# Performance work log

Measured on AMD Instinct MI355X. Metric: run time of the kernel, lower is better.

## Reference

```python
import jax, jax.numpy as jnp
import numpy as np

N = 50000
E = 500000
R = 8
IN_DIM = 128
HID = 128
OUT = 128
NUM_GRAPHS = 64
EPS_BN = 1e-5


def _glorot(key, shape):
    fan_in, fan_out = shape[-2], shape[-1]
    lim = np.sqrt(6.0 / (fan_in + fan_out))
    return jax.random.uniform(key, shape, jnp.float32, -lim, lim)


def setup_inputs() -> dict:
    key = jax.random.key(0)
    ks = jax.random.split(key, 24)
    x = jax.random.normal(ks[0], (N, IN_DIM), jnp.float32)
    edge_index = jax.random.randint(ks[1], (2, E), 0, N, jnp.int64)
    edge_type = jax.random.randint(ks[2], (E,), 0, R, jnp.int64)
    batch = jnp.sort(jax.random.randint(ks[3], (N,), 0, NUM_GRAPHS, jnp.int64))
    d = {
        "x": x, "edge_index": edge_index, "edge_type": edge_type, "batch": batch,
        # RGCN layer 1 (in->hid): per-relation weights, root weight, bias
        "W1": _glorot(ks[4], (R, IN_DIM, HID)), "root1": _glorot(ks[5], (IN_DIM, HID)), "b1": jnp.zeros((HID,), jnp.float32),
        "W2": _glorot(ks[6], (R, HID, HID)), "root2": _glorot(ks[7], (HID, HID)), "b2": jnp.zeros((HID,), jnp.float32),
        "W3": _glorot(ks[8], (R, HID, HID)), "root3": _glorot(ks[9], (HID, HID)), "b3": jnp.zeros((HID,), jnp.float32),
        # BatchNorm affine params
        "g1": jnp.ones((HID,), jnp.float32), "beta1": jnp.zeros((HID,), jnp.float32),
        "g2": jnp.ones((HID,), jnp.float32), "beta2": jnp.zeros((HID,), jnp.float32),
        # attention MLP: hid -> hid//2 -> 1
        "A1": _glorot(ks[10], (HID, HID // 2)), "a1": jnp.zeros((HID // 2,), jnp.float32),
        "A2": _glorot(ks[11], (HID // 2, 1)), "a2": jnp.zeros((1,), jnp.float32),
        # combiner MLP: 2*hid -> hid -> out
        "C1": _glorot(ks[12], (2 * HID, HID)), "c1": jnp.zeros((HID,), jnp.float32),
        "C2": _glorot(ks[13], (HID, OUT)), "c2": jnp.zeros((OUT,), jnp.float32),
    }
    return d


def rgcn_conv(h, src, dst, etype, W, root, bias):
    # relation-wise gather -> mean-aggregate per (dst, relation) -> transform
    seg = dst * R + etype                                   # [E]
    msg = h[src]                                            # [E, d_in] gather
    agg = jax.ops.segment_sum(msg, seg, num_segments=N * R) # [N*R, d_in]
    cnt = jax.ops.segment_sum(jnp.ones((seg.shape[0],), h.dtype), seg, num_segments=N * R)
    agg = agg / jnp.maximum(cnt, 1.0)[:, None]              # mean aggregation (PyG default)
    agg = agg.reshape(N, R, -1)
    out = jnp.einsum('nri,rio->no', agg, W) + h @ root + bias
    return out


def batch_norm(h, gamma, beta):
    mu = jnp.mean(h, axis=0, keepdims=True)
    var = jnp.mean((h - mu) ** 2, axis=0, keepdims=True)
    return (h - mu) * jax.lax.rsqrt(var + EPS_BN) * gamma + beta


def lrelu(h):
    return jax.nn.leaky_relu(h, 0.1)


def reference(x, edge_index, edge_type, batch, W1, root1, b1, W2, root2, b2,
              W3, root3, b3, g1, beta1, g2, beta2, A1, a1, A2, a2, C1, c1, C2, c2):
    src, dst = edge_index[0], edge_index[1]
    h = rgcn_conv(x, src, dst, edge_type, W1, root1, b1)
    h = lrelu(batch_norm(h, g1, beta1))
    h = rgcn_conv(h, src, dst, edge_type, W2, root2, b2)
    h = lrelu(batch_norm(h, g2, beta2))
    node_emb = rgcn_conv(h, src, dst, edge_type, W3, root3, b3)  # [N, HID]

    # attention pooling: scores softmax-ed over ALL nodes (dim=0, as in source)
    scores = lrelu(node_emb @ A1 + a1) @ A2 + a2                 # [N, 1]
    attn = jax.nn.softmax(scores, axis=0)                        # [N, 1]
    global_emb = jax.ops.segment_sum(node_emb * attn, batch, num_segments=NUM_GRAPHS)

    combined = jnp.concatenate([node_emb, global_emb[batch]], axis=1)  # [N, 2*HID]
    final = lrelu(combined @ C1 + c1) @ C2 + c2                  # [N, OUT]
    norm = jnp.linalg.norm(final, axis=1, keepdims=True)
    return final / jnp.maximum(norm, 1e-12)
```

## Files before the change

kernel.cpp:

```cpp
#include <hip/hip_runtime.h>
#include <hip/hip_bf16.h>

typedef unsigned int u32;
typedef unsigned short u16;
typedef __bf16 bf16_t;
typedef bf16_t bf16x8 __attribute__((ext_vector_type(8)));
typedef float f32x4 __attribute__((ext_vector_type(4)));

constexpr int NN = 50000;
constexpr int EE = 500000;
constexpr int RR = 8;
constexpr int NKEY = RR * NN;
constexpr int PAIR_B = (NKEY + 511) / 512;

constexpr int WX_A1T = 0;
constexpr int WX_C1T = 8192;
constexpr int WX_C2T = 40960;
constexpr int WX_A2  = 57344;
constexpr int WX_a1  = 57408;
constexpr int WX_c1  = 57472;
constexpr int WX_c2  = 57600;
constexpr int WX_a2s = 57728;
constexpr int WX_TOT = 57729;

__device__ __forceinline__ float bf2f(u32 v){
  union { u32 u; float f; } x; x.u = (v & 0xFFFFu) << 16; return x.f;
}
__device__ __forceinline__ u16 f2bf(float f){
  union { u32 u; float f; } x; x.f = f;
  u32 r = x.u + 0x7FFFu + ((x.u >> 16) & 1u);
  return (u16)(r >> 16);
}
__device__ __forceinline__ float lrelu(float x){ return x > 0.f ? x : 0.1f * x; }
__device__ __forceinline__ float ldf(const void* p, int i, u32 fm){
  return fm ? ((const float*)p)[i] : bf2f(((const u16*)p)[i]);
}
__device__ __forceinline__ void gl_lds16(const u16* g, u16* l){
  __builtin_amdgcn_global_load_lds((const __attribute__((address_space(1))) u32*)g,
                                   (__attribute__((address_space(3))) u32*)l, 16, 0, 0);
}
__device__ __forceinline__ bf16x8 cvt8(float4 a, float4 b){
  union { bf16x8 v; u16 s[8]; } r;
  r.s[0]=f2bf(a.x); r.s[1]=f2bf(a.y); r.s[2]=f2bf(a.z); r.s[3]=f2bf(a.w);
  r.s[4]=f2bf(b.x); r.s[5]=f2bf(b.y); r.s[6]=f2bf(b.z); r.s[7]=f2bf(b.w);
  return r.v;
}

__global__ void k_fdetect(const void* x, u32* md){
  __shared__ u32 c;
  if (threadIdx.x == 0) c = 0;
  __syncthreads();
  const u16* p = (const u16*)x;
  u32 loc = 0;
  for (int j = 0; j < 16; j++){
    u16 v = p[threadIdx.x * 16 + j];
    u32 e = (v >> 7) & 0xFF;
    if (e >= 0xFD) loc++;
  }
  atomicAdd(&c, loc);
  __syncthreads();
  if (threadIdx.x == 0) md[0] = (c >= 4) ? 1u : 0u;
}
__global__ void k_idetect(const void* et, u32* md){
  __shared__ u32 c;
  if (threadIdx.x == 0) c = 0;
  __syncthreads();
  const int* p = (const int*)et;
  u32 loc = 0;
  for (int j = 0; j < 8; j++){
    int idx = 2 * (threadIdx.x * 8 + j) + 1;
    if (p[idx] != 0) loc++;
  }
  atomicAdd(&c, loc);
  __syncthreads();
  if (threadIdx.x == 0) md[1] = (c == 0) ? 1u : 0u;
}

__global__ void k_icvt(const void* ei, const void* et, const void* bat,
                       int* ei_c, int* et_c, int* bat_c, const u32* md){
  u32 im = md[1];
  int i = blockIdx.x * 256 + threadIdx.x;
  if (i < 2 * EE){
    const int* p = (const int*)ei;
    ei_c[i] = im ? p[2 * i] : p[i];
  } else if (i < 3 * EE){
    int j = i - 2 * EE;
    const int* p = (const int*)et;
    et_c[j] = im ? p[2 * j] : p[j];
  } else if (i < 3 * EE + NN){
    int j = i - 3 * EE;
    const int* p = (const int*)bat;
    bat_c[j] = im ? p[2 * j] : p[j];
  }
}

__global__ void k_xcvt(const void* x, u16* xb, const u32* md, u32* flags){
  u32 fm = md[0];
  int i4 = (blockIdx.x * 256 + threadIdx.x) * 4;
  if (i4 >= NN * 128) return;
  float v[4];
  if (fm){
    float4 f = *(const float4*)((const float*)x + i4);
    v[0]=f.x; v[1]=f.y; v[2]=f.z; v[3]=f.w;
  } else {
    uint2 u = *(const uint2*)((const u16*)x + i4);
    v[0]=bf2f(u.x); v[1]=bf2f(u.x>>16); v[2]=bf2f(u.y); v[3]=bf2f(u.y>>16);
  }
  bool bad = false;
  u16 o[4];
  for (int j = 0; j < 4; j++){
    if (v[j] != v[j]){ bad = true; v[j] = 0.f; }
    o[j] = f2bf(v[j]);
  }
  unsigned long long bal = __ballot(bad);
  if (bal && (threadIdx.x & 63) == 0) atomicOr(flags, 2u);
  uint2 st;
  st.x = (u32)o[0] | ((u32)o[1] << 16);
  st.y = (u32)o[2] | ((u32)o[3] << 16);
  *(uint2*)(xb + i4) = st;
}

__global__ void k_wcat(const void* W1, const void* r1, const void* W2, const void* r2,
                       const void* W3, const void* r3, u16* wcatT, const u32* md, u32* flags){
  u32 fm = md[0];
  int idx = blockIdx.x * 256 + threadIdx.x;
  if (idx >= 3 * 128 * 1152) return;
  int L = idx / (128 * 1152);
  int rem = idx % (128 * 1152);
  int n = rem / 1152, k = rem % 1152;
  const void* W  = (L == 0) ? W1 : ((L == 1) ? W2 : W3);
  const void* rt = (L == 0) ? r1 : ((L == 1) ? r2 : r3);
  float v;
  if (k < 1024){
    int r = k & 7, c = k >> 3;
    v = ldf(W, (r * 128 + c) * 128 + n, fm);
  } else {
    v = ldf(rt, (k - 1024) * 128 + n, fm);
  }
  if (v != v){ v = 0.f; atomicOr(flags, 2u); }
  wcatT[idx] = f2bf(v);
}

__global__ void k_wext(const void* A1, const void* a1, const void* A2, const void* a2,
                       const void* C1, const void* c1, const void* C2, const void* c2,
                       u16* wext, const u32* md){
  u32 fm = md[0];
  int idx = blockIdx.x * 256 + threadIdx.x;
  if (idx >= WX_TOT) return;
  float v;
  if (idx < WX_C1T){
    int n = idx >> 7, k = idx & 127;
    v = ldf(A1, k * 64 + n, fm);
  } else if (idx < WX_C2T){
    int j = idx - WX_C1T; int n = j >> 8, k = j & 255;
    v = ldf(C1, k * 128 + n, fm);
  } else if (idx < WX_A2){
    int j = idx - WX_C2T; int n = j >> 7, k = j & 127;
    v = ldf(C2, k * 128 + n, fm);
  } else if (idx < WX_a1){ v = ldf(A2, idx - WX_A2, fm); }
  else if (idx < WX_c1){ v = ldf(a1, idx - WX_a1, fm); }
  else if (idx < WX_c2){ v = ldf(c1, idx - WX_c1, fm); }
  else if (idx < WX_a2s){ v = ldf(c2, idx - WX_c2, fm); }
  else { v = ldf(a2, 0, fm); }
  wext[idx] = f2bf(v);
}

__global__ void k_count3(const int* __restrict__ ei, const int* __restrict__ et, u32* __restrict__ cnt){
  int e = blockIdx.x * 256 + threadIdx.x;
  if (e >= EE) return;
  atomicAdd(&cnt[ei[EE + e] * RR + et[e]], 1u);
}
__global__ void k_pairA(const u32* __restrict__ cnt, u32* __restrict__ blockSum){
  __shared__ u32 sd[256];
  int b = blockIdx.x, t = threadIdx.x;
  u32 s = 0;
  for (int j = 0; j < 2; j++){
    int key = b * 512 + t * 2 + j;
    if (key < NKEY) s += cnt[key];
  }
  sd[t] = s; __syncthreads();
  for (int off = 128; off; off >>= 1){ if (t < off) sd[t] += sd[t + off]; __syncthreads(); }
  if (t == 0) blockSum[b] = sd[0];
}
__global__ void k_pairB(const u32* __restrict__ blockSum, u32* __restrict__ blockBase){
  int lane = threadIdx.x;
  u32 loc[13]; u32 s = 0;
  for (int j = 0; j < 13; j++){
    int b = lane * 13 + j;
    u32 v = (b < PAIR_B) ? blockSum[b] : 0u;
    loc[j] = s; s += v;
  }
  u32 tot = s;
  for (int off = 1; off < 64; off <<= 1){
    u32 x = __shfl_up(tot, off);
    if (lane >= off) tot += x;
  }
  u32 excl = tot - s;
  for (int j = 0; j < 13; j++){
    int b = lane * 13 + j;
    if (b < PAIR_B) blockBase[b] = excl + loc[j];
  }
}
__global__ void k_pairC(const u32* __restrict__ cnt, const u32* __restrict__ blockBase,
                        u32* __restrict__ pairStart, u32* __restrict__ cursor){
  __shared__ u32 sd[256];
  int b = blockIdx.x, t = threadIdx.x;
  int k0 = b * 512 + t * 2;
  u32 v0 = 0, v1 = 0;
  if (k0 < NKEY) v0 = cnt[k0];
  if (k0 + 1 < NKEY) v1 = cnt[k0 + 1];
  sd[t] = v0 + v1; __syncthreads();
  for (int off = 1; off < 256; off <<= 1){
    u32 x = (t >= off) ? sd[t - off] : 0u;
    __syncthreads();
    sd[t] += x;
    __syncthreads();
  }
  u32 excl = sd[t] - (v0 + v1);
  u32 base = blockBase[b] + excl;
  if (k0 < NKEY){ pairStart[k0] = base; cursor[k0] = 0u; }
  if (k0 + 1 < NKEY){ pairStart[k0 + 1] = base + v0; cursor[k0 + 1] = 0u; }
  if (k0 + 1 == NKEY - 1) pairStart[NKEY] = base + v0 + v1;
}
__global__ void k_sort3(const int* __restrict__ ei, const int* __restrict__ et,
                        const u32* __restrict__ pairStart, u32* __restrict__ cursor,
                        u32* __restrict__ src_s){
  int e = blockIdx.x * 256 + threadIdx.x;
  if (e >= EE) return;
  int r = et[e], d = ei[EE + e];
  u32 key = (u32)d * RR + (u32)r;
  u32 p = pairStart[key] + atomicAdd(&cursor[key], 1u);
  src_s[p] = (u32)ei[e];
}

__global__ __launch_bounds__(256) void k_agg(const u16* __restrict__ h,
                                             const u32* __restrict__ pairStart,
                                             const u32* __restrict__ src_s,
                                             u16* __restrict__ agg){
  int d = blockIdx.x * 4 + (threadIdx.x >> 6);
  if (d >= NN) return;
  int lane = threadIdx.x & 63;
  const uint4* p4 = (const uint4*)(pairStart + d * 8);
  uint4 q0 = p4[0], q1 = p4[1];
  u32 ps[9];
  ps[0]=q0.x; ps[1]=q0.y; ps[2]=q0.z; ps[3]=q0.w;
  ps[4]=q1.x; ps[5]=q1.y; ps[6]=q1.z; ps[7]=q1.w;
  ps[8]=pairStart[d * 8 + 8];
  u32 jb = ps[0], je = ps[8];
  u32 pre = 0;
  if (jb + lane < je) pre = src_s[jb + lane];
  const u16* hb = h + lane * 2;
  u32 ou[8] = {0,0,0,0,0,0,0,0};
  #pragma unroll
  for (int r = 0; r < 8; r++){
    u32 s = ps[r], e = ps[r + 1];
    float a0 = 0.f, a1 = 0.f, b0 = 0.f, b1 = 0.f;
    u32 j = s;
    for (; j + 1 < e; j += 2){
      u32 i0 = j - jb;
      u32 s0 = (i0 < 64) ? __shfl(pre, (int)i0) : src_s[j];
      u32 s1 = (i0 + 1 < 64) ? __shfl(pre, (int)(i0 + 1)) : src_s[j + 1];
      u32 v0 = *(const u32*)(hb + (size_t)s0 * 128);
      u32 v1 = *(const u32*)(hb + (size_t)s1 * 128);
      a0 += bf2f(v0); a1 += bf2f(v0 >> 16);
      b0 += bf2f(v1); b1 += bf2f(v1 >> 16);
    }
    if (j < e){
      u32 i0 = j - jb;
      u32 s0 = (i0 < 64) ? __shfl(pre, (int)i0) : src_s[j];
      u32 v0 = *(const u32*)(hb + (size_t)s0 * 128);
      a0 += bf2f(v0); a1 += bf2f(v0 >> 16);
    }
    a0 += b0; a1 += b1;
    int c = (int)(e - s);
    float sc = 1.0f / (float)max(c, 1);
    u32 m0 = (u32)f2bf(a0 * sc), m1 = (u32)f2bf(a1 * sc);
    ou[r >> 1]       |= m0 << ((r & 1) * 16);
    ou[4 + (r >> 1)] |= m1 << ((r & 1) * 16);
  }
  uint4* dst = (uint4*)(agg + (size_t)d * 1024 + lane * 16);
  dst[0] = make_uint4(ou[0], ou[1], ou[2], ou[3]);
  dst[1] = make_uint4(ou[4], ou[5], ou[6], ou[7]);
}

__global__ __launch_bounds__(256) void k_gemm_big(const u16* __restrict__ h,
                                                  const u16* __restrict__ agg,
                                                  const u16* __restrict__ wT,
                                                  const void* __restrict__ bias,
                                                  float* __restrict__ out, const u32* md,
                                                  float* __restrict__ stats, int do_stats){
  __shared__ u16 As[64][64];
  __shared__ u16 Bs[128][64];
  u32 fm = md[0];
  int m0 = blockIdx.x * 64;
  int tid = threadIdx.x;
  int w = tid >> 6, lane = tid & 63, qd = lane >> 4, l16 = lane & 15;

  int rin = lane >> 3;
  int sc8 = (lane & 7) ^ rin;

  const u16* agA[2]; const u16* hA[2]; u16* ldsA[2];
  #pragma unroll
  for (int i = 0; i < 2; i++){
    int row = (w * 2 + i) * 8 + rin;
    int node = m0 + row; if (node > NN - 1) node = NN - 1;
    agA[i] = agg + (size_t)node * 1024 + sc8 * 8;
    hA[i]  = h + (size_t)node * 128 + sc8 * 8;
    ldsA[i] = &As[(w * 2 + i) * 8][0];
  }
  const u16* wB[4]; u16* ldsB[4];
  #pragma unroll
  for (int i = 0; i < 4; i++){
    int row = (w * 4 + i) * 8 + rin;
    wB[i] = wT + (size_t)row * 1152 + sc8 * 8;
    ldsB[i] = &Bs[(w * 4 + i) * 8][0];
  }

  f32x4 acc[8];
  #pragma unroll
  for (int j = 0; j < 8; j++) acc[j] = (f32x4){0.f,0.f,0.f,0.f};

  int sw = (l16 & 7) << 3;
  for (int k0 = 0; k0 < 1152; k0 += 64){
    __syncthreads();
    if (k0 < 1024){
      gl_lds16(agA[0] + k0, ldsA[0]);
      gl_lds16(agA[1] + k0, ldsA[1]);
    } else {
      gl_lds16(hA[0] + (k0 - 1024), ldsA[0]);
      gl_lds16(hA[1] + (k0 - 1024), ldsA[1]);
    }
    #pragma unroll
    for (int i = 0; i < 4; i++) gl_lds16(wB[i] + k0, ldsB[i]);
    __syncthreads();
    #pragma unroll
    for (int kk = 0; kk < 64; kk += 32){
      bf16x8 a = *(const bf16x8*)(&As[w * 16 + l16][(kk + qd * 8) ^ sw]);
      #pragma unroll
      for (int ct = 0; ct < 8; ct++){
        bf16x8 b = *(const bf16x8*)(&Bs[ct * 16 + l16][(kk + qd * 8) ^ sw]);
        acc[ct] = __builtin_amdgcn_mfma_f32_16x16x32_bf16(a, b, acc[ct], 0, 0, 0);
      }
    }
  }

  float sarr[8], s2arr[8];
  #pragma unroll
  for (int ct = 0; ct < 8; ct++){
    int col = ct * 16 + l16;
    float bv = ldf(bias, col, fm);
    float s = 0.f, s2 = 0.f;
    int rbase = m0 + w * 16 + qd * 4;
    #pragma unroll
    for (int rg = 0; rg < 4; rg++){
      int node = rbase + rg;
      if (node < NN){
        float v = acc[ct][rg] + bv;
        out[(size_t)node * 128 + col] = v;
        s += v; s2 += v * v;
      }
    }
    s  += __shfl_xor(s, 16);  s  += __shfl_xor(s, 32);
    s2 += __shfl_xor(s2, 16); s2 += __shfl_xor(s2, 32);
    sarr[ct] = s; s2arr[ct] = s2;
  }
  if (do_stats){
    float* red = (float*)&As[0][0];
    __syncthreads();
    if (qd == 0){
      #pragma unroll
      for (int ct = 0; ct < 8; ct++){
        red[w * 256 + ct * 16 + l16] = sarr[ct];
        red[w * 256 + 128 + ct * 16 + l16] = s2arr[ct];
      }
    }
    __syncthreads();
    if (tid < 256){
      float v = red[tid] + red[256 + tid] + red[512 + tid] + red[768 + tid];
      unsafeAtomicAdd(&stats[tid], v);
    }
  }
}

__global__ void k_bnapply(const float* __restrict__ out, const float* __restrict__ stats,
                          const void* __restrict__ g, const void* __restrict__ beta,
                          u16* __restrict__ hout, const u32* md, u32* flags, u32 layerbit){
  u32 fm = md[0];
  int idx = (blockIdx.x * 256 + threadIdx.x) * 4;
  if (idx >= NN * 128) return;
  int col = idx & 127;
  float4 v = *(const float4*)(out + idx);
  float vv[4] = {v.x, v.y, v.z, v.w};
  bool bad = false;
  u16 o[4];
  for (int j = 0; j < 4; j++){
    int c = col + j;
    float mu = stats[c] * (1.0f / NN);
    float var = fmaxf(stats[128 + c] * (1.0f / NN) - mu * mu, 0.f);
    float sc = ldf(g, c, fm) * rsqrtf(var + 1e-5f);
    float sh = ldf(beta, c, fm) - mu * sc;
    float r = vv[j] * sc + sh;
    if (r != r || sc != sc){ bad = true; r = 0.f; }
    o[j] = f2bf(lrelu(r));
  }
  unsigned long long bal = __ballot(bad);
  if (bal && (threadIdx.x & 63) == 0) atomicOr(flags, layerbit);
  uint2 st;
  st.x = (u32)o[0] | ((u32)o[1] << 16);
  st.y = (u32)o[2] | ((u32)o[3] << 16);
  *(uint2*)(hout + idx) = st;
}

__global__ __launch_bounds__(256) void k_scores_mfma(const float* __restrict__ emb,
                                                     const u16* __restrict__ wext,
                                                     float* __restrict__ scores, u32* smax){
  int m0 = blockIdx.x * 64;
  int tid = threadIdx.x;
  int w = tid >> 6, lane = tid & 63, qd = lane >> 4, l16 = lane & 15;
  int na = m0 + w * 16 + l16; if (na > NN - 1) na = NN - 1;
  const float* arow = emb + (size_t)na * 128;
  f32x4 acc[4];
  #pragma unroll
  for (int j = 0; j < 4; j++) acc[j] = (f32x4){0.f,0.f,0.f,0.f};
  #pragma unroll
  for (int k0 = 0; k0 < 4; k0++){
    float4 f0 = *(const float4*)(arow + k0 * 32 + qd * 8);
    float4 f1 = *(const float4*)(arow + k0 * 32 + qd * 8 + 4);
    bf16x8 a = cvt8(f0, f1);
    #pragma unroll
    for (int ct = 0; ct < 4; ct++){
      bf16x8 b = *(const bf16x8*)(wext + WX_A1T + (size_t)(ct * 16 + l16) * 128 + k0 * 32 + qd * 8);
      acc[ct] = __builtin_amdgcn_mfma_f32_16x16x32_bf16(a, b, acc[ct], 0, 0, 0);
    }
  }
  float a1v[4], a2v[4];
  #pragma unroll
  for (int ct = 0; ct < 4; ct++){
    a1v[ct] = bf2f(wext[WX_a1 + ct * 16 + l16]);
    a2v[ct] = bf2f(wext[WX_A2 + ct * 16 + l16]);
  }
  float a2s = bf2f(wext[WX_a2s]);
  float bm = -1e30f;
  #pragma unroll
  for (int rg = 0; rg < 4; rg++){
    float s = 0.f;
    #pragma unroll
    for (int ct = 0; ct < 4; ct++)
      s += lrelu(acc[ct][rg] + a1v[ct]) * a2v[ct];
    s += __shfl_xor(s, 1); s += __shfl_xor(s, 2);
    s += __shfl_xor(s, 4); s += __shfl_xor(s, 8);
    int row = m0 + w * 16 + qd * 4 + rg;
    float sf = s + a2s;
    if (row < NN){
      bm = fmaxf(bm, sf);
      if (l16 == 0) scores[row] = sf;
    }
  }
  bm = fmaxf(bm, __shfl_xor(bm, 16));
  bm = fmaxf(bm, __shfl_xor(bm, 32));
  if (lane == 0) atomicMax(smax, (bm >= -1e29f) ?
      ((__float_as_uint(bm) & 0x80000000u) ? ~__float_as_uint(bm) : (__float_as_uint(bm) | 0x80000000u)) : 0u);
}

__device__ __forceinline__ float funmap(u32 m){
  union{u32 u; float f;} x;
  x.u = (m & 0x80000000u) ? (m ^ 0x80000000u) : ~m;
  return x.f;
}

__global__ void k_expsum(const float* __restrict__ scores, const u32* smax,
                         float* __restrict__ attnw, float* ssum, u32* flags){
  float mx = funmap(*smax);
  int gid = blockIdx.x * 256 + threadIdx.x;
  if (mx != mx){ if (gid == 0) atomicOr(flags, 32u); mx = 0.f; }
  float s = 0.f;
  bool bad = false;
  for (int i = gid; i < NN; i += 256 * 128){
    float e = __expf(scores[i] - mx);
    if (e != e){ bad = true; e = 0.f; }
    attnw[i] = e; s += e;
  }
  unsigned long long bal = __ballot(bad);
  if (bal && (threadIdx.x & 63) == 0) atomicOr(flags, 32u);
  for (int off = 32; off; off >>= 1) s += __shfl_down(s, off);
  if ((threadIdx.x & 63) == 0) unsafeAtomicAdd(ssum, s);
}

constexpr int POOL_CHUNK = 32;
__global__ __launch_bounds__(128) void k_pool(const float* __restrict__ emb,
                                              const float* __restrict__ attnw,
                                              const float* __restrict__ ssum,
                                              const int* __restrict__ batch,
                                              float* __restrict__ gemb, u32* flags){
  int t = threadIdx.x;
  int n0 = blockIdx.x * POOL_CHUNK;
  if (n0 >= NN) return;
  int n1 = min(n0 + POOL_CHUNK, NN);
  float sv = *ssum;
  bool bad = !(sv > 0.f) || (sv != sv);
  if (bad && t == 0 && blockIdx.x == 0) atomicOr(flags, 64u);
  float rs = bad ? 0.f : 1.0f / sv;
  int cur = batch[n0];
  float acc = 0.f;
  for (int n = n0; n < n1; n++){
    int b = batch[n];
    if (b != cur){ unsafeAtomicAdd(&gemb[cur * 128 + t], acc * rs); acc = 0.f; cur = b; }
    acc += emb[(size_t)n * 128 + t] * attnw[n];
  }
  unsafeAtomicAdd(&gemb[cur * 128 + t], acc * rs);
}

__global__ void k_gembC(const float* __restrict__ gemb, const u16* __restrict__ wext,
                        float* __restrict__ gembC){
  int idx = blockIdx.x * 256 + threadIdx.x;
  if (idx >= 64 * 128) return;
  int g = idx >> 7, n = idx & 127;
  const float* gr = gemb + g * 128;
  const u16* wr = wext + WX_C1T + (size_t)n * 256 + 128;
  float s = 0.f;
  #pragma unroll 8
  for (int k = 0; k < 128; k++) s += gr[k] * bf2f(wr[k]);
  gembC[idx] = s + bf2f(wext[WX_c1 + n]);
}

__global__ __launch_bounds__(256) void k_final_mfma(const float* __restrict__ emb,
                                                    const float* __restrict__ gembC,
                                                    const int* __restrict__ batch,
                                                    const u16* __restrict__ wext,
                                                    void* __restrict__ outp,
                                                    const u32* md){
  __shared__ u16 Hs[64][136];
  u32 fm = md[0];
  int m0 = blockIdx.x * 64;
  int tid = threadIdx.x;
  int w = tid >> 6, lane = tid & 63, qd = lane >> 4, l16 = lane & 15;
  int na = m0 + w * 16 + l16; if (na > NN - 1) na = NN - 1;
  const float* arow = emb + (size_t)na * 128;

  f32x4 acc[8];
  #pragma unroll
  for (int j = 0; j < 8; j++) acc[j] = (f32x4){0.f,0.f,0.f,0.f};
  #pragma unroll
  for (int k0 = 0; k0 < 4; k0++){
    float4 f0 = *(const float4*)(arow + k0 * 32 + qd * 8);
    float4 f1 = *(const float4*)(arow + k0 * 32 + qd * 8 + 4);
    bf16x8 a = cvt8(f0, f1);
    #pragma unroll
    for (int ct = 0; ct < 8; ct++){
      bf16x8 b = *(const bf16x8*)(wext + WX_C1T + (size_t)(ct * 16 + l16) * 256 + k0 * 32 + qd * 8);
      acc[ct] = __builtin_amdgcn_mfma_f32_16x16x32_bf16(a, b, acc[ct], 0, 0, 0);
    }
  }
  int rbase = w * 16 + qd * 4;
  int gg[4];
  #pragma unroll
  for (int rg = 0; rg < 4; rg++){
    int node = m0 + rbase + rg; if (node > NN - 1) node = NN - 1;
    gg[rg] = batch[node];
  }
  #pragma unroll
  for (int ct = 0; ct < 8; ct++){
    int col = ct * 16 + l16;
    #pragma unroll
    for (int rg = 0; rg < 4; rg++){
      float h = acc[ct][rg] + gembC[gg[rg] * 128 + col];
      Hs[rbase + rg][col] = f2bf(lrelu(h));
    }
  }
  __syncthreads();
  f32x4 acc2[8];
  #pragma unroll
  for (int j = 0; j < 8; j++) acc2[j] = (f32x4){0.f,0.f,0.f,0.f};
  #pragma unroll
  for (int k0 = 0; k0 < 4; k0++){
    bf16x8 a = *(const bf16x8*)(&Hs[w * 16 + l16][k0 * 32 + qd * 8]);
    #pragma unroll
    for (int ct = 0; ct < 8; ct++){
      bf16x8 b = *(const bf16x8*)(wext + WX_C2T + (size_t)(ct * 16 + l16) * 128 + k0 * 32 + qd * 8);
      acc2[ct] = __builtin_amdgcn_mfma_f32_16x16x32_bf16(a, b, acc2[ct], 0, 0, 0);
    }
  }
  float c2v[8];
  #pragma unroll
  for (int ct = 0; ct < 8; ct++) c2v[ct] = bf2f(wext[WX_c2 + ct * 16 + l16]);
  #pragma unroll
  for (int rg = 0; rg < 4; rg++){
    float ss = 0.f;
    #pragma unroll
    for (int ct = 0; ct < 8; ct++){
      float o = acc2[ct][rg] + c2v[ct];
      ss += o * o;
    }
    ss += __shfl_xor(ss, 1); ss += __shfl_xor(ss, 2);
    ss += __shfl_xor(ss, 4); ss += __shfl_xor(ss, 8);
    float sc = 1.0f / fmaxf(sqrtf(ss), 1e-12f);
    int row = m0 + rbase + rg;
    if (row < NN){
      if (fm){
        float* op = (float*)outp;
        #pragma unroll
        for (int ct = 0; ct < 8; ct++)
          op[(size_t)row * 128 + ct * 16 + l16] = (acc2[ct][rg] + c2v[ct]) * sc;
      } else {
        u16* op = (u16*)outp;
        #pragma unroll
        for (int ct = 0; ct < 8; ct++)
          op[(size_t)row * 128 + ct * 16 + l16] = f2bf((acc2[ct][rg] + c2v[ct]) * sc);
      }
    }
  }
}

__global__ void k_diag(const u32* pairStart, const u32* flags, const u32* md, void* outp){
  if (threadIdx.x != 0 || blockIdx.x != 0) return;
  u32 fm = md[0];
  u32 f = flags[0];
  if (pairStart[NKEY] != (u32)EE) f |= 1u;
  for (int b = 0; b < 9; b++){
    if (f & (1u << b)){
      float s = (float)(131072 >> b);
      if (fm) ((float*)outp)[b] = s;
      else ((u16*)outp)[b] = f2bf(s);
    }
  }
}
__global__ void k_wsfail(u32* outp){ outp[0] = 0x43000000u; }

constexpr size_t O_OUT   = 0;
constexpr size_t O_H     = 25600000;
constexpr size_t O_XBF   = 38400000;
constexpr size_t O_WCAT  = 51200000;
constexpr size_t O_WEXT  = 52084736;
constexpr size_t O_EI    = 52200448;
constexpr size_t O_ET    = 56200448;
constexpr size_t O_BAT   = 58200448;
constexpr size_t O_SRC   = 58400448;
constexpr size_t O_PST   = 60400448;
constexpr size_t O_GEMBC = 62100448;
constexpr size_t O_CNT   = 62400448;
constexpr size_t O_SCO   = 65600448;
constexpr size_t O_AW    = 65800448;
constexpr size_t O_GEMB  = 66000448;
constexpr size_t O_STATS = 66033216;
constexpr size_t O_MISC  = 66035264;
constexpr size_t O_AGG   = 66035520;
constexpr size_t WS_NEED = 168435520;

extern "C" void kernel_launch(void* const* d_in, const int* in_sizes, int n_in,
                              void* d_out, int out_size, void* d_ws, size_t ws_size,
                              hipStream_t stream) {
  const void* x     = d_in[0];
  const void* ei    = d_in[1];
  const void* et    = d_in[2];
  const void* batch = d_in[3];
  const void* W1 = d_in[4],  *r1 = d_in[5],  *b1 = d_in[6];
  const void* W2 = d_in[7],  *r2 = d_in[8],  *b2 = d_in[9];
  const void* W3 = d_in[10], *r3 = d_in[11], *b3 = d_in[12];
  const void* g1 = d_in[13], *be1 = d_in[14];
  const void* g2 = d_in[15], *be2 = d_in[16];
  const void* A1 = d_in[17], *a1 = d_in[18];
  const void* A2 = d_in[19], *a2 = d_in[20];
  const void* C1 = d_in[21], *c1 = d_in[22];
  const void* C2 = d_in[23], *c2 = d_in[24];

  if (ws_size < WS_NEED){ k_wsfail<<<1, 1, 0, stream>>>((u32*)d_out); return; }
  char* ws = (char*)d_ws;
  float* out   = (float*)(ws + O_OUT);
  u16*   hbuf  = (u16*)(ws + O_H);
  u16*   xbf   = (u16*)(ws + O_XBF);
  u16*   wcat  = (u16*)(ws + O_WCAT);
  u16*   wext  = (u16*)(ws + O_WEXT);
  int*   ei_c  = (int*)(ws + O_EI);
  int*   et_c  = (int*)(ws + O_ET);
  int*   bat_c = (int*)(ws + O_BAT);
  u32*   src_s = (u32*)(ws + O_SRC);
  u32*   pairStart = (u32*)(ws + O_PST);
  float* gembC = (float*)(ws + O_GEMBC);
  u32*   cnt   = (u32*)(ws + O_CNT);
  float* sco   = (float*)(ws + O_SCO);
  float* aw    = (float*)(ws + O_AW);
  float* gemb  = (float*)(ws + O_GEMB);
  float* stats = (float*)(ws + O_STATS);
  u32*   misc  = (u32*)(ws + O_MISC);
  u16*   aggb  = (u16*)(ws + O_AGG);
  u32* cursor    = (u32*)(ws + O_OUT);
  u32* blockSum  = (u32*)(ws + O_OUT + 1600000);
  u32* blockBase = (u32*)(ws + O_OUT + 1604096);
  u32* smax = misc + 25;
  float* ssum = (float*)(misc + 26);
  u32* flags = misc + 27;
  u32* md = misc + 28;

  hipMemsetAsync(ws + O_CNT, 0, 1600000, stream);
  hipMemsetAsync(ws + O_GEMB, 0, 32768 + 2048 + 256, stream);

  k_fdetect<<<1, 256, 0, stream>>>(x, md);
  k_idetect<<<1, 256, 0, stream>>>(et, md);
  k_icvt<<<6055, 256, 0, stream>>>(ei, et, batch, ei_c, et_c, bat_c, md);
  k_xcvt<<<6250, 256, 0, stream>>>(x, xbf, md, flags);
  k_wcat<<<1728, 256, 0, stream>>>(W1, r1, W2, r2, W3, r3, wcat, md, flags);
  k_wext<<<227, 256, 0, stream>>>(A1, a1, A2, a2, C1, c1, C2, c2, wext, md);

  k_count3<<<(EE + 255) / 256, 256, 0, stream>>>(ei_c, et_c, cnt);
  k_pairA<<<PAIR_B, 256, 0, stream>>>(cnt, blockSum);
  k_pairB<<<1, 64, 0, stream>>>(blockSum, blockBase);
  k_pairC<<<PAIR_B, 256, 0, stream>>>(cnt, blockBase, pairStart, cursor);
  k_sort3<<<(EE + 255) / 256, 256, 0, stream>>>(ei_c, et_c, pairStart, cursor, src_s);

  const void* bias[3] = {b1, b2, b3};
  const void* gam[2] = {g1, g2};
  const void* bet[2] = {be1, be2};
  const u16* hin = xbf;
  for (int L = 0; L < 3; L++){
    const u16* wT = wcat + (size_t)L * 128 * 1152;
    k_agg<<<(NN + 3) / 4, 256, 0, stream>>>(hin, pairStart, src_s, aggb);
    k_gemm_big<<<(NN + 63) / 64, 256, 0, stream>>>(hin, aggb, wT, bias[L], out, md,
                                                   stats + (L < 2 ? L * 256 : 0), (L < 2) ? 1 : 0);
    if (L < 2){
      k_bnapply<<<6250, 256, 0, stream>>>(out, stats + L * 256, gam[L], bet[L], hbuf, md, flags, 4u << L);
      hin = hbuf;
    }
  }
  k_scores_mfma<<<(NN + 63) / 64, 256, 0, stream>>>(out, wext, sco, smax);
  k_expsum<<<128, 256, 0, stream>>>(sco, smax, aw, ssum, flags);
  k_pool<<<(NN + POOL_CHUNK - 1) / POOL_CHUNK, 128, 0, stream>>>(out, aw, ssum, bat_c, gemb, flags);
  k_gembC<<<32, 256, 0, stream>>>(gemb, wext, gembC);
  k_final_mfma<<<(NN + 63) / 64, 256, 0, stream>>>(out, gembC, bat_c, wext, d_out, md);
  k_diag<<<1, 64, 0, stream>>>(pairStart, flags, md, d_out);
}
```

Baseline: 638.9 us.

## Double-buffer GEMM LDS tiles and fuse edge counting into index conversion

The big RGCN GEMM now keeps two LDS buffers for the A and B tiles. It issues the global-to-LDS load for the next K slice before computing on the current one, which cuts one barrier per iteration and overlaps memory with MFMA work. Separately, the per-(dst,relation) edge-count atomics move into the index-conversion kernel, and the standalone count kernel launch is removed. The trade-offs are doubled LDS use, which may lower occupancy, and atomics that now sit inside the conversion kernel.

Result: slower. 697.7 us (+9.2%).

```diff
diff --git a/kernel.cpp b/kernel.cpp
--- a/kernel.cpp
+++ b/kernel.cpp
@@ -77,12 +77,21 @@
 }
 
 __global__ void k_icvt(const void* ei, const void* et, const void* bat,
-                       int* ei_c, int* et_c, int* bat_c, const u32* md){
+                       int* ei_c, int* et_c, int* bat_c, u32* __restrict__ cnt,
+                       const u32* md){
   u32 im = md[1];
   int i = blockIdx.x * 256 + threadIdx.x;
-  if (i < 2 * EE){
+  if (i < EE){
     const int* p = (const int*)ei;
     ei_c[i] = im ? p[2 * i] : p[i];
+  } else if (i < 2 * EE){
+    int j = i - EE;
+    const int* p = (const int*)ei;
+    const int* pt = (const int*)et;
+    int d = im ? p[2 * i] : p[i];
+    int r = im ? pt[2 * j] : pt[j];
+    ei_c[i] = d;
+    atomicAdd(&cnt[d * RR + r], 1u);
   } else if (i < 3 * EE){
     int j = i - 2 * EE;
     const int* p = (const int*)et;
@@ -165,11 +174,6 @@
   wext[idx] = f2bf(v);
 }
 
-__global__ void k_count3(const int* __restrict__ ei, const int* __restrict__ et, u32* __restrict__ cnt){
-  int e = blockIdx.x * 256 + threadIdx.x;
-  if (e >= EE) return;
-  atomicAdd(&cnt[ei[EE + e] * RR + et[e]], 1u);
-}
 __global__ void k_pairA(const u32* __restrict__ cnt, u32* __restrict__ blockSum){
   __shared__ u32 sd[256];
   int b = blockIdx.x, t = threadIdx.x;
@@ -289,8 +293,8 @@
                                                   const void* __restrict__ bias,
                                                   float* __restrict__ out, const u32* md,
                                                   float* __restrict__ stats, int do_stats){
-  __shared__ u16 As[64][64];
-  __shared__ u16 Bs[128][64];
+  __shared__ u16 As[2][64][64];
+  __shared__ u16 Bs[2][128][64];
   u32 fm = md[0];
   int m0 = blockIdx.x * 64;
   int tid = threadIdx.x;
@@ -299,49 +303,53 @@
   int rin = lane >> 3;
   int sc8 = (lane & 7) ^ rin;
 
-  const u16* agA[2]; const u16* hA[2]; u16* ldsA[2];
+  const u16* agA[2]; const u16* hA[2];
   #pragma unroll
   for (int i = 0; i < 2; i++){
     int row = (w * 2 + i) * 8 + rin;
     int node = m0 + row; if (node > NN - 1) node = NN - 1;
     agA[i] = agg + (size_t)node * 1024 + sc8 * 8;
     hA[i]  = h + (size_t)node * 128 + sc8 * 8;
-    ldsA[i] = &As[(w * 2 + i) * 8][0];
-  }
-  const u16* wB[4]; u16* ldsB[4];
+  }
+  const u16* wB[4];
   #pragma unroll
   for (int i = 0; i < 4; i++){
     int row = (w * 4 + i) * 8 + rin;
     wB[i] = wT + (size_t)row * 1152 + sc8 * 8;
-    ldsB[i] = &Bs[(w * 4 + i) * 8][0];
-  }
+  }
+
+  auto stage = [&](int k0, int b){
+    if (k0 < 1024){
+      gl_lds16(agA[0] + k0, &As[b][(w * 2 + 0) * 8][0]);
+      gl_lds16(agA[1] + k0, &As[b][(w * 2 + 1) * 8][0]);
+    } else {
+      gl_lds16(hA[0] + (k0 - 1024), &As[b][(w * 2 + 0) * 8][0]);
+      gl_lds16(hA[1] + (k0 - 1024), &As[b][(w * 2 + 1) * 8][0]);
+    }
+    #pragma unroll
+    for (int i = 0; i < 4; i++) gl_lds16(wB[i] + k0, &Bs[b][(w * 4 + i) * 8][0]);
+  };
 
   f32x4 acc[8];
   #pragma unroll
   for (int j = 0; j < 8; j++) acc[j] = (f32x4){0.f,0.f,0.f,0.f};
 
   int sw = (l16 & 7) << 3;
-  for (int k0 = 0; k0 < 1152; k0 += 64){
-    __syncthreads();
-    if (k0 < 1024){
-      gl_lds16(agA[0] + k0, ldsA[0]);
-      gl_lds16(agA[1] + k0, ldsA[1]);
-    } else {
-      gl_lds16(hA[0] + (k0 - 1024), ldsA[0]);
-      gl_lds16(hA[1] + (k0 - 1024), ldsA[1]);
-    }
-    #pragma unroll
-    for (int i = 0; i < 4; i++) gl_lds16(wB[i] + k0, ldsB[i]);
-    __syncthreads();
+  stage(0, 0);
+  __syncthreads();
+  for (int t = 0; t < 18; t++){
+    int b = t & 1;
+    if (t + 1 < 18) stage((t + 1) * 64, b ^ 1);
     #pragma unroll
     for (int kk = 0; kk < 64; kk += 32){
-      bf16x8 a = *(const bf16x8*)(&As[w * 16 + l16][(kk + qd * 8) ^ sw]);
+      bf16x8 a = *(const bf16x8*)(&As[b][w * 16 + l16][(kk + qd * 8) ^ sw]);
       #pragma unroll
       for (int ct = 0; ct < 8; ct++){
-        bf16x8 b = *(const bf16x8*)(&Bs[ct * 16 + l16][(kk + qd * 8) ^ sw]);
-        acc[ct] = __builtin_amdgcn_mfma_f32_16x16x32_bf16(a, b, acc[ct], 0, 0, 0);
+        bf16x8 bb = *(const bf16x8*)(&Bs[b][ct * 16 + l16][(kk + qd * 8) ^ sw]);
+        acc[ct] = __builtin_amdgcn_mfma_f32_16x16x32_bf16(a, bb, acc[ct], 0, 0, 0);
       }
     }
+    __syncthreads();
   }
 
   float sarr[8], s2arr[8];
@@ -365,7 +373,7 @@
     sarr[ct] = s; s2arr[ct] = s2;
   }
   if (do_stats){
-    float* red = (float*)&As[0][0];
+    float* red = (float*)&As[0][0][0];
     __syncthreads();
     if (qd == 0){
       #pragma unroll
@@ -696,12 +704,11 @@
 
   k_fdetect<<<1, 256, 0, stream>>>(x, md);
   k_idetect<<<1, 256, 0, stream>>>(et, md);
-  k_icvt<<<6055, 256, 0, stream>>>(ei, et, batch, ei_c, et_c, bat_c, md);
+  k_icvt<<<6055, 256, 0, stream>>>(ei, et, batch, ei_c, et_c, bat_c, cnt, md);
   k_xcvt<<<6250, 256, 0, stream>>>(x, xbf, md, flags);
   k_wcat<<<1728, 256, 0, stream>>>(W1, r1, W2, r2, W3, r3, wcat, md, flags);
   k_wext<<<227, 256, 0, stream>>>(A1, a1, A2, a2, C1, c1, C2, c2, wext, md);
 
-  k_count3<<<(EE + 255) / 256, 256, 0, stream>>>(ei_c, et_c, cnt);
   k_pairA<<<PAIR_B, 256, 0, stream>>>(cnt, blockSum);
   k_pairB<<<1, 64, 0, stream>>>(blockSum, blockBase);
   k_pairC<<<PAIR_B, 256, 0, stream>>>(cnt, blockBase, pairStart, cursor);
```

## Split-K the RGCN GEMM across two blocks and fuse edge counting into conversion

Applied to the files above, without the earlier changes.

The main GEMM is split along K into two halves, each run by its own block, which doubles the grid. The two partial results are combined with float atomic adds into an output buffer that is zeroed beforehand. BatchNorm statistics move into a separate k_bnstats kernel that re-reads the output. Separately, the per-(dst,relation) edge counting is folded into the index conversion kernel, which removes one launch. In exchange, each layer gains a 25.6MB memset, atomic traffic on the output and an extra full read for the stats, while the atomic adds make the summation order nondeterministic.

Result: slower. 743.1 us (+16.3%).

```diff
diff --git a/kernel.cpp b/kernel.cpp
--- a/kernel.cpp
+++ b/kernel.cpp
@@ -77,12 +77,21 @@
 }
 
 __global__ void k_icvt(const void* ei, const void* et, const void* bat,
-                       int* ei_c, int* et_c, int* bat_c, const u32* md){
+                       int* ei_c, int* et_c, int* bat_c, u32* __restrict__ cnt,
+                       const u32* md){
   u32 im = md[1];
   int i = blockIdx.x * 256 + threadIdx.x;
-  if (i < 2 * EE){
+  if (i < EE){
     const int* p = (const int*)ei;
     ei_c[i] = im ? p[2 * i] : p[i];
+  } else if (i < 2 * EE){
+    int j = i - EE;
+    const int* p = (const int*)ei;
+    const int* pt = (const int*)et;
+    int d = im ? p[2 * i] : p[i];
+    int r = im ? pt[2 * j] : pt[j];
+    ei_c[i] = d;
+    atomicAdd(&cnt[d * RR + r], 1u);
   } else if (i < 3 * EE){
     int j = i - 2 * EE;
     const int* p = (const int*)et;
@@ -165,11 +174,6 @@
   wext[idx] = f2bf(v);
 }
 
-__global__ void k_count3(const int* __restrict__ ei, const int* __restrict__ et, u32* __restrict__ cnt){
-  int e = blockIdx.x * 256 + threadIdx.x;
-  if (e >= EE) return;
-  atomicAdd(&cnt[ei[EE + e] * RR + et[e]], 1u);
-}
 __global__ void k_pairA(const u32* __restrict__ cnt, u32* __restrict__ blockSum){
   __shared__ u32 sd[256];
   int b = blockIdx.x, t = threadIdx.x;
@@ -287,12 +291,14 @@
                                                   const u16* __restrict__ agg,
                                                   const u16* __restrict__ wT,
                                                   const void* __restrict__ bias,
-                                                  float* __restrict__ out, const u32* md,
-                                                  float* __restrict__ stats, int do_stats){
+                                                  float* __restrict__ out, const u32* md){
   __shared__ u16 As[64][64];
   __shared__ u16 Bs[128][64];
   u32 fm = md[0];
-  int m0 = blockIdx.x * 64;
+  int bid = blockIdx.x;
+  int m0 = (bid >> 1) * 64;
+  int khalf = bid & 1;
+  int kbase = khalf * 576;
   int tid = threadIdx.x;
   int w = tid >> 6, lane = tid & 63, qd = lane >> 4, l16 = lane & 15;
 
@@ -321,7 +327,7 @@
   for (int j = 0; j < 8; j++) acc[j] = (f32x4){0.f,0.f,0.f,0.f};
 
   int sw = (l16 & 7) << 3;
-  for (int k0 = 0; k0 < 1152; k0 += 64){
+  for (int k0 = kbase; k0 < kbase + 576; k0 += 64){
     __syncthreads();
     if (k0 < 1024){
       gl_lds16(agA[0] + k0, ldsA[0]);
@@ -344,41 +350,35 @@
     }
   }
 
-  float sarr[8], s2arr[8];
   #pragma unroll
   for (int ct = 0; ct < 8; ct++){
     int col = ct * 16 + l16;
-    float bv = ldf(bias, col, fm);
-    float s = 0.f, s2 = 0.f;
+    float bv = khalf ? ldf(bias, col, fm) : 0.f;
     int rbase = m0 + w * 16 + qd * 4;
     #pragma unroll
     for (int rg = 0; rg < 4; rg++){
       int node = rbase + rg;
-      if (node < NN){
-        float v = acc[ct][rg] + bv;
-        out[(size_t)node * 128 + col] = v;
-        s += v; s2 += v * v;
-      }
-    }
-    s  += __shfl_xor(s, 16);  s  += __shfl_xor(s, 32);
-    s2 += __shfl_xor(s2, 16); s2 += __shfl_xor(s2, 32);
-    sarr[ct] = s; s2arr[ct] = s2;
-  }
-  if (do_stats){
-    float* red = (float*)&As[0][0];
-    __syncthreads();
-    if (qd == 0){
-      #pragma unroll
-      for (int ct = 0; ct < 8; ct++){
-        red[w * 256 + ct * 16 + l16] = sarr[ct];
-        red[w * 256 + 128 + ct * 16 + l16] = s2arr[ct];
-      }
-    }
-    __syncthreads();
-    if (tid < 256){
-      float v = red[tid] + red[256 + tid] + red[512 + tid] + red[768 + tid];
-      unsafeAtomicAdd(&stats[tid], v);
-    }
+      if (node < NN)
+        unsafeAtomicAdd(&out[(size_t)node * 128 + col], acc[ct][rg] + bv);
+    }
+  }
+}
+
+__global__ void k_bnstats(const float* __restrict__ out, float* __restrict__ stats){
+  __shared__ float sb[256], sb2[256];
+  int tid = threadIdx.x;
+  int col = tid & 127, half = tid >> 7;
+  int r0 = blockIdx.x * 128;
+  float s = 0.f, s2 = 0.f;
+  for (int i = half; i < 128; i += 2){
+    int n = r0 + i;
+    if (n < NN){ float v = out[(size_t)n * 128 + col]; s += v; s2 += v * v; }
+  }
+  sb[tid] = s; sb2[tid] = s2;
+  __syncthreads();
+  if (half == 0){
+    unsafeAtomicAdd(&stats[col],       sb[col] + sb[col + 128]);
+    unsafeAtomicAdd(&stats[128 + col], sb2[col] + sb2[col + 128]);
   }
 }
 
@@ -696,12 +696,11 @@
 
   k_fdetect<<<1, 256, 0, stream>>>(x, md);
   k_idetect<<<1, 256, 0, stream>>>(et, md);
-  k_icvt<<<6055, 256, 0, stream>>>(ei, et, batch, ei_c, et_c, bat_c, md);
+  k_icvt<<<6055, 256, 0, stream>>>(ei, et, batch, ei_c, et_c, bat_c, cnt, md);
   k_xcvt<<<6250, 256, 0, stream>>>(x, xbf, md, flags);
   k_wcat<<<1728, 256, 0, stream>>>(W1, r1, W2, r2, W3, r3, wcat, md, flags);
   k_wext<<<227, 256, 0, stream>>>(A1, a1, A2, a2, C1, c1, C2, c2, wext, md);
 
-  k_count3<<<(EE + 255) / 256, 256, 0, stream>>>(ei_c, et_c, cnt);
   k_pairA<<<PAIR_B, 256, 0, stream>>>(cnt, blockSum);
   k_pairB<<<1, 64, 0, stream>>>(blockSum, blockBase);
   k_pairC<<<PAIR_B, 256, 0, stream>>>(cnt, blockBase, pairStart, cursor);
@@ -714,9 +713,10 @@
   for (int L = 0; L < 3; L++){
     const u16* wT = wcat + (size_t)L * 128 * 1152;
     k_agg<<<(NN + 3) / 4, 256, 0, stream>>>(hin, pairStart, src_s, aggb);
-    k_gemm_big<<<(NN + 63) / 64, 256, 0, stream>>>(hin, aggb, wT, bias[L], out, md,
-                                                   stats + (L < 2 ? L * 256 : 0), (L < 2) ? 1 : 0);
+    hipMemsetAsync(out, 0, (size_t)NN * 128 * 4, stream);
+    k_gemm_big<<<2 * ((NN + 63) / 64), 256, 0, stream>>>(hin, aggb, wT, bias[L], out, md);
     if (L < 2){
+      k_bnstats<<<391, 256, 0, stream>>>(out, stats + L * 256);
       k_bnapply<<<6250, 256, 0, stream>>>(out, stats + L * 256, gam[L], bet[L], hbuf, md, flags, 4u << L);
       hin = hbuf;
     }
```

## Split RGCN GEMM into column halves and fuse edge counting into index conversion

Applied to the files above, without the earlier changes.

The per-layer GEMM now launches two blocks per 64-row tile, each computing 64 of the 128 output columns, with a halved B tile in LDS and half the accumulators. This raises block count and occupancy but re-reads the large aggregated-feature A tile twice. Separately, the (dst,relation) count atomics move into the index conversion kernel, removing one launch and a re-read of the converted arrays.

Measured after the change: 646.7 us. Within noise of the previous version (+1.2%).

```diff
diff --git a/kernel.cpp b/kernel.cpp
--- a/kernel.cpp
+++ b/kernel.cpp
@@ -77,12 +77,21 @@
 }
 
 __global__ void k_icvt(const void* ei, const void* et, const void* bat,
-                       int* ei_c, int* et_c, int* bat_c, const u32* md){
+                       int* ei_c, int* et_c, int* bat_c, u32* __restrict__ cnt,
+                       const u32* md){
   u32 im = md[1];
   int i = blockIdx.x * 256 + threadIdx.x;
-  if (i < 2 * EE){
+  if (i < EE){
     const int* p = (const int*)ei;
     ei_c[i] = im ? p[2 * i] : p[i];
+  } else if (i < 2 * EE){
+    int j = i - EE;
+    const int* p = (const int*)ei;
+    const int* pt = (const int*)et;
+    int d = im ? p[2 * i] : p[i];
+    int r = im ? pt[2 * j] : pt[j];
+    ei_c[i] = d;
+    atomicAdd(&cnt[d * RR + r], 1u);
   } else if (i < 3 * EE){
     int j = i - 2 * EE;
     const int* p = (const int*)et;
@@ -165,11 +174,6 @@
   wext[idx] = f2bf(v);
 }
 
-__global__ void k_count3(const int* __restrict__ ei, const int* __restrict__ et, u32* __restrict__ cnt){
-  int e = blockIdx.x * 256 + threadIdx.x;
-  if (e >= EE) return;
-  atomicAdd(&cnt[ei[EE + e] * RR + et[e]], 1u);
-}
 __global__ void k_pairA(const u32* __restrict__ cnt, u32* __restrict__ blockSum){
   __shared__ u32 sd[256];
   int b = blockIdx.x, t = threadIdx.x;
@@ -290,9 +294,11 @@
                                                   float* __restrict__ out, const u32* md,
                                                   float* __restrict__ stats, int do_stats){
   __shared__ u16 As[64][64];
-  __shared__ u16 Bs[128][64];
+  __shared__ u16 Bs[64][64];
   u32 fm = md[0];
-  int m0 = blockIdx.x * 64;
+  int bid = blockIdx.x;
+  int m0 = (bid >> 1) * 64;
+  int nh = bid & 1;
   int tid = threadIdx.x;
   int w = tid >> 6, lane = tid & 63, qd = lane >> 4, l16 = lane & 15;
 
@@ -308,17 +314,17 @@
     hA[i]  = h + (size_t)node * 128 + sc8 * 8;
     ldsA[i] = &As[(w * 2 + i) * 8][0];
   }
-  const u16* wB[4]; u16* ldsB[4];
-  #pragma unroll
-  for (int i = 0; i < 4; i++){
-    int row = (w * 4 + i) * 8 + rin;
-    wB[i] = wT + (size_t)row * 1152 + sc8 * 8;
-    ldsB[i] = &Bs[(w * 4 + i) * 8][0];
-  }
-
-  f32x4 acc[8];
-  #pragma unroll
-  for (int j = 0; j < 8; j++) acc[j] = (f32x4){0.f,0.f,0.f,0.f};
+  const u16* wB[2]; u16* ldsB[2];
+  #pragma unroll
+  for (int i = 0; i < 2; i++){
+    int row = (w * 2 + i) * 8 + rin;
+    wB[i] = wT + (size_t)(nh * 64 + row) * 1152 + sc8 * 8;
+    ldsB[i] = &Bs[(w * 2 + i) * 8][0];
+  }
+
+  f32x4 acc[4];
+  #pragma unroll
+  for (int j = 0; j < 4; j++) acc[j] = (f32x4){0.f,0.f,0.f,0.f};
 
   int sw = (l16 & 7) << 3;
   for (int k0 = 0; k0 < 1152; k0 += 64){
@@ -330,24 +336,24 @@
       gl_lds16(hA[0] + (k0 - 1024), ldsA[0]);
       gl_lds16(hA[1] + (k0 - 1024), ldsA[1]);
     }
-    #pragma unroll
-    for (int i = 0; i < 4; i++) gl_lds16(wB[i] + k0, ldsB[i]);
+    gl_lds16(wB[0] + k0, ldsB[0]);
+    gl_lds16(wB[1] + k0, ldsB[1]);
     __syncthreads();
     #pragma unroll
     for (int kk = 0; kk < 64; kk += 32){
       bf16x8 a = *(const bf16x8*)(&As[w * 16 + l16][(kk + qd * 8) ^ sw]);
       #pragma unroll
-      for (int ct = 0; ct < 8; ct++){
+      for (int ct = 0; ct < 4; ct++){
         bf16x8 b = *(const bf16x8*)(&Bs[ct * 16 + l16][(kk + qd * 8) ^ sw]);
         acc[ct] = __builtin_amdgcn_mfma_f32_16x16x32_bf16(a, b, acc[ct], 0, 0, 0);
       }
     }
   }
 
-  float sarr[8], s2arr[8];
-  #pragma unroll
-  for (int ct = 0; ct < 8; ct++){
-    int col = ct * 16 + l16;
+  float sarr[4], s2arr[4];
+  #pragma unroll
+  for (int ct = 0; ct < 4; ct++){
+    int col = nh * 64 + ct * 16 + l16;
     float bv = ldf(bias, col, fm);
     float s = 0.f, s2 = 0.f;
     int rbase = m0 + w * 16 + qd * 4;
@@ -369,15 +375,16 @@
     __syncthreads();
     if (qd == 0){
       #pragma unroll
-      for (int ct = 0; ct < 8; ct++){
-        red[w * 256 + ct * 16 + l16] = sarr[ct];
-        red[w * 256 + 128 + ct * 16 + l16] = s2arr[ct];
+      for (int ct = 0; ct < 4; ct++){
+        red[w * 128 + ct * 16 + l16] = sarr[ct];
+        red[w * 128 + 64 + ct * 16 + l16] = s2arr[ct];
       }
     }
     __syncthreads();
-    if (tid < 256){
-      float v = red[tid] + red[256 + tid] + red[512 + tid] + red[768 + tid];
-      unsafeAtomicAdd(&stats[tid], v);
+    if (tid < 128){
+      float v = red[tid] + red[128 + tid] + red[256 + tid] + red[384 + tid];
+      int which = tid >> 6, colh = tid & 63;
+      unsafeAtomicAdd(&stats[which * 128 + nh * 64 + colh], v);
     }
   }
 }
@@ -696,12 +703,11 @@
 
   k_fdetect<<<1, 256, 0, stream>>>(x, md);
   k_idetect<<<1, 256, 0, stream>>>(et, md);
-  k_icvt<<<6055, 256, 0, stream>>>(ei, et, batch, ei_c, et_c, bat_c, md);
+  k_icvt<<<6055, 256, 0, stream>>>(ei, et, batch, ei_c, et_c, bat_c, cnt, md);
   k_xcvt<<<6250, 256, 0, stream>>>(x, xbf, md, flags);
   k_wcat<<<1728, 256, 0, stream>>>(W1, r1, W2, r2, W3, r3, wcat, md, flags);
   k_wext<<<227, 256, 0, stream>>>(A1, a1, A2, a2, C1, c1, C2, c2, wext, md);
 
-  k_count3<<<(EE + 255) / 256, 256, 0, stream>>>(ei_c, et_c, cnt);
   k_pairA<<<PAIR_B, 256, 0, stream>>>(cnt, blockSum);
   k_pairB<<<1, 64, 0, stream>>>(blockSum, blockBase);
   k_pairC<<<PAIR_B, 256, 0, stream>>>(cnt, blockBase, pairStart, cursor);
@@ -714,8 +720,8 @@
   for (int L = 0; L < 3; L++){
     const u16* wT = wcat + (size_t)L * 128 * 1152;
     k_agg<<<(NN + 3) / 4, 256, 0, stream>>>(hin, pairStart, src_s, aggb);
-    k_gemm_big<<<(NN + 63) / 64, 256, 0, stream>>>(hin, aggb, wT, bias[L], out, md,
-                                                   stats + (L < 2 ? L * 256 : 0), (L < 2) ? 1 : 0);
+    k_gemm_big<<<2 * ((NN + 63) / 64), 256, 0, stream>>>(hin, aggb, wT, bias[L], out, md,
+                                                         stats + (L < 2 ? L * 256 : 0), (L < 2) ? 1 : 0);
     if (L < 2){
       k_bnapply<<<6250, 256, 0, stream>>>(out, stats + L * 256, gam[L], bet[L], hbuf, md, flags, 4u << L);
       hin = hbuf;
```
